# Optimization experiments

Measured on AMD Instinct MI355X. Metric: run time of the kernel, lower is better.

Reference implementation:

```python
import jax, jax.numpy as jnp
import numpy as np

H = 128
W = 128
TILE = 32
N = 12000
BIG = 1e30


def _render(means2D, cov2d, color, opacity, depths):
    # pixel coords, indexing='xy': pix[y, x] = (x, y)
    pix = jnp.stack(jnp.meshgrid(jnp.arange(W), jnp.arange(H), indexing='xy'), axis=-1).astype(means2D.dtype)
    c00 = cov2d[:, 0, 0]; c01 = cov2d[:, 0, 1]; c10 = cov2d[:, 1, 0]; c11 = cov2d[:, 1, 1]
    det = c00 * c11 - c01 * c10
    # get_radius (no_grad in torch)
    mid = 0.5 * (c00 + c11)
    s = jnp.sqrt(jnp.maximum(mid * mid - det, 0.1))
    radii = jax.lax.stop_gradient(3.0 * jnp.ceil(jnp.sqrt(jnp.maximum(mid + s, mid - s))))
    # get_rect, clipped to image bounds
    rmin = jnp.clip(means2D - radii[:, None], 0.0, W - 1.0)  # H == W == 128
    rmax = jnp.clip(means2D + radii[:, None], 0.0, W - 1.0)
    rmin = jax.lax.stop_gradient(rmin)
    rmax = jax.lax.stop_gradient(rmax)
    # closed-form 2x2 inverse (conic)
    inv_det = 1.0 / det
    conic = jnp.stack([jnp.stack([c11, -c01], axis=-1),
                       jnp.stack([-c10, c00], axis=-1)], axis=-2) * inv_det[:, None, None]

    img_c = jnp.ones((H, W, 3), means2D.dtype)
    img_d = jnp.zeros((H, W, 1), means2D.dtype)
    img_a = jnp.zeros((H, W, 1), means2D.dtype)

    for h in range(0, H, TILE):
        for w in range(0, W, TILE):
            tlx = jnp.maximum(rmin[:, 0], w); tly = jnp.maximum(rmin[:, 1], h)
            brx = jnp.minimum(rmax[:, 0], w + TILE - 1.0); bry = jnp.minimum(rmax[:, 1], h + TILE - 1.0)
            mask = (brx > tlx) & (bry > tly)  # [N]
            # depth sort with non-intersecting gaussians pushed to the back
            order = jnp.argsort(jnp.where(mask, depths, BIG))
            sm = means2D[order]          # [N,2]
            sc = conic[order]            # [N,2,2]
            so = opacity[order]          # [N,1]
            scol = color[order]          # [N,3]
            smask = mask[order]
            sd = jnp.where(smask, depths[order], 0.0)
            tile_coord = pix[h:h + TILE, w:w + TILE].reshape(-1, 2)  # [1024,2]
            dx = tile_coord[:, None, :] - sm[None]                   # [1024,N,2]
            gw = jnp.exp(-0.5 * (dx[..., 0] ** 2 * sc[:, 0, 0]
                                 + dx[..., 1] ** 2 * sc[:, 1, 1]
                                 + dx[..., 0] * dx[..., 1] * (sc[:, 0, 1] + sc[:, 1, 0])))
            alpha = gw[..., None] * so[None] * smask[None, :, None].astype(gw.dtype)  # [1024,N,1]
            alpha = jnp.minimum(alpha, 0.99)
            T = jnp.cumprod(jnp.concatenate([jnp.ones_like(alpha[:, :1]), 1.0 - alpha[:, :-1]], axis=1), axis=1)
            wgt = T * alpha
            acc = wgt.sum(axis=1)                                   # [1024,1]
            tc = (wgt * scol[None]).sum(axis=1) + (1.0 - acc)       # white background
            td = (wgt * sd[None, :, None]).sum(axis=1)
            img_c = img_c.at[h:h + TILE, w:w + TILE].set(tc.reshape(TILE, TILE, 3))
            img_d = img_d.at[h:h + TILE, w:w + TILE].set(td.reshape(TILE, TILE, 1))
            img_a = img_a.at[h:h + TILE, w:w + TILE].set(acc.reshape(TILE, TILE, 1))
    return img_c, img_d, img_a


def setup_inputs() -> dict:
    key = jax.random.key(0)
    k1, k2, k3, k4, k5 = jax.random.split(key, 5)
    means2D = jax.random.uniform(k1, (N, 2), jnp.float32) * 128.0
    L = 0.6 * jax.random.normal(k2, (N, 2, 2), jnp.float32)
    cov2d = L @ jnp.swapaxes(L, -1, -2) + 0.3 * jnp.eye(2, dtype=jnp.float32)[None]
    color = jax.random.uniform(k3, (N, 3), jnp.float32)
    opacity = jax.random.uniform(k4, (N, 1), jnp.float32)
    depths = jax.random.uniform(k5, (N,), jnp.float32) * 10.0 + 0.2
    return {"means2D": means2D, "cov2d": cov2d, "color": color, "opacity": opacity, "depths": depths}


def reference(means2D, cov2d, color, opacity, depths):
    return _render(means2D, cov2d, color, opacity, depths)
```

## Files before the change

kernel.cpp:

```cpp
#include <hip/hip_runtime.h>
#include <stdint.h>

#define HH 128
#define WW 128
#define NTILES 16
#define NPIX (HH * WW)
#define MAXSEG 16
#define JCH 1024

__global__ void k0_init(const float* __restrict__ depths,
                        uint64_t* __restrict__ keys,
                        int* __restrict__ rank, int N) {
    int i = blockIdx.x * blockDim.x + threadIdx.x;
    if (i < N) {
        rank[i] = 0;
        keys[i] = ((uint64_t)__float_as_uint(depths[i]) << 32) | (uint64_t)i;
    }
}

__global__ __launch_bounds__(256) void k1_rank(const uint64_t* __restrict__ keys,
                                               int* __restrict__ rank,
                                               int N, int ncj) {
    int bi = blockIdx.x / ncj;
    int bj = blockIdx.x % ncj;
    int t  = threadIdx.x;
    int i  = bi * 256 + t;
    uint64_t ki = (i < N) ? keys[i] : 0;

    int j0   = bj * JCH;
    int jend = min(N, j0 + JCH);

    int c0 = 0, c1 = 0, c2 = 0, c3 = 0;
    int j = j0;
    for (; j + 4 <= jend; j += 4) {
        uint64_t a = keys[j + 0];
        uint64_t b = keys[j + 1];
        uint64_t c = keys[j + 2];
        uint64_t d = keys[j + 3];
        c0 += (a < ki);
        c1 += (b < ki);
        c2 += (c < ki);
        c3 += (d < ki);
    }
    for (; j < jend; j++) c0 += (keys[j] < ki);

    if (i < N) {
        int cnt = (c0 + c1) + (c2 + c3);
        if (cnt) atomicAdd(&rank[i], cnt);
    }
}

__global__ __launch_bounds__(256) void k2_scatter(const float* __restrict__ means,
                                                  const float* __restrict__ cov,
                                                  const float* __restrict__ color,
                                                  const float* __restrict__ opac,
                                                  const float* __restrict__ depths,
                                                  const int* __restrict__ rank,
                                                  float* __restrict__ sorted,
                                                  int* __restrict__ smask,
                                                  int N) {
    int i = blockIdx.x * blockDim.x + threadIdx.x;
    if (i >= N) return;

    float mx = means[2 * i + 0];
    float my = means[2 * i + 1];
    float c00 = cov[4 * i + 0];
    float c01 = cov[4 * i + 1];
    float c10 = cov[4 * i + 2];
    float c11 = cov[4 * i + 3];

    float det = c00 * c11 - c01 * c10;
    float mid = 0.5f * (c00 + c11);
    float s = sqrtf(fmaxf(mid * mid - det, 0.1f));
    float radii = 3.0f * ceilf(sqrtf(fmaxf(mid + s, mid - s)));

    float rminx = fminf(fmaxf(mx - radii, 0.0f), (float)(WW - 1));
    float rminy = fminf(fmaxf(my - radii, 0.0f), (float)(HH - 1));
    float rmaxx = fminf(fmaxf(mx + radii, 0.0f), (float)(WW - 1));
    float rmaxy = fminf(fmaxf(my + radii, 0.0f), (float)(HH - 1));

    float inv_det = 1.0f / det;
    float A = c11 * inv_det;
    float B = c00 * inv_det;
    float C = -(c01 + c10) * inv_det;

    int bits = 0;
    for (int ty = 0; ty < 4; ty++) {
        float h = (float)(ty * 32);
        float tly = fmaxf(rminy, h);
        float bry = fminf(rmaxy, h + 31.0f);
        bool yok = bry > tly;
        for (int tx = 0; tx < 4; tx++) {
            float w = (float)(tx * 32);
            float tlx = fmaxf(rminx, w);
            float brx = fminf(rmaxx, w + 31.0f);
            if (yok && (brx > tlx)) bits |= 1 << (ty * 4 + tx);
        }
    }

    int r = rank[i];
    float4* g4 = (float4*)(sorted + (size_t)r * 12);
    g4[0] = make_float4(mx, my, A, B);
    g4[1] = make_float4(C, opac[i], color[3 * i + 0], color[3 * i + 1]);
    g4[2] = make_float4(color[3 * i + 2], depths[i], 0.0f, 0.0f);
    smask[r] = bits;
}

__global__ __launch_bounds__(256) void k3_compact(const int* __restrict__ smask,
                                                  int* __restrict__ lists,
                                                  int* __restrict__ counts,
                                                  int N) {
    int tile = blockIdx.x;
    int t = threadIdx.x;
    int lane = t & 63;
    int wv = t >> 6;

    __shared__ int wsum[4];
    __shared__ int s_run;
    if (t == 0) s_run = 0;
    __syncthreads();

    int* list = lists + (size_t)tile * N;

    for (int base = 0; base < N; base += 256) {
        int idx = base + t;
        int flag = (idx < N) ? ((smask[idx] >> tile) & 1) : 0;
        unsigned long long bal = __ballot(flag);
        int pre = __popcll(bal & ((lane == 0) ? 0ull : ((1ull << lane) - 1ull)));
        int wtot = __popcll(bal);
        if (lane == 0) wsum[wv] = wtot;
        __syncthreads();
        int woff = 0;
        for (int q = 0; q < wv; q++) woff += wsum[q];
        int run = s_run;
        if (flag) list[run + woff + pre] = idx;
        __syncthreads();
        if (t == 0) s_run = run + wsum[0] + wsum[1] + wsum[2] + wsum[3];
        __syncthreads();
    }
    if (t == 0) counts[tile] = s_run;
}

#define CH 64
__global__ __launch_bounds__(256) void k4_render(const float* __restrict__ sorted,
                                                 const int* __restrict__ lists,
                                                 const int* __restrict__ counts,
                                                 float4* __restrict__ part4,
                                                 float2* __restrict__ part2,
                                                 int N, int S) {
    int b = blockIdx.x;
    int s = b & (S - 1);
    int q = b / S;
    int tile = q >> 2;
    int sub = q & 3;
    int tx = tile & 3;
    int ty = tile >> 2;
    int t = threadIdx.x;

    int p = sub * 256 + t;
    int px = p & 31;
    int py = p >> 5;
    float fx = (float)(tx * 32 + px);
    float fy = (float)(ty * 32 + py);

    int cnt = counts[tile];
    int chunk = (cnt + S - 1) / S;
    int beg = s * chunk;
    int end = min(cnt, beg + chunk);
    const int* list = lists + (size_t)tile * N;

    __shared__ __align__(16) float4 s_g[CH * 3];
    __shared__ int s_idx[CH];

    float T = 1.0f;
    float ar = 0.0f, ag = 0.0f, ab = 0.0f, ad = 0.0f, aa = 0.0f;

    for (int base = beg; base < end; base += CH) {
        int m = min(CH, end - base);
        if (t < CH) s_idx[t] = (t < m) ? list[base + t] : 0;
        __syncthreads();
        if (t < m * 3) {
            int k = t / 3;
            int c = t - k * 3;
            s_g[t] = ((const float4*)(sorted + (size_t)s_idx[k] * 12))[c];
        }
        __syncthreads();
        for (int k = 0; k < m; k++) {
            float4 ga = s_g[k * 3 + 0];
            float4 gb = s_g[k * 3 + 1];
            float4 gc = s_g[k * 3 + 2];
            float dx = fx - ga.x;
            float dy = fy - ga.y;
            float e = ga.z * dx * dx + ga.w * dy * dy + gb.x * dx * dy;
            float gw = __expf(-0.5f * e);
            float alpha = fminf(gw * gb.y, 0.99f);
            float w = T * alpha;
            ar += w * gb.z;
            ag += w * gb.w;
            ab += w * gc.x;
            ad += w * gc.y;
            aa += w;
            T *= (1.0f - alpha);
        }
        __syncthreads();
    }

    size_t o = (size_t)s * NPIX + (size_t)tile * 1024 + p;
    part4[o] = make_float4(ar, ag, ab, ad);
    part2[o] = make_float2(aa, T);
}

__global__ __launch_bounds__(256) void k5_combine(const float4* __restrict__ part4,
                                                  const float2* __restrict__ part2,
                                                  float* __restrict__ out, int S) {
    int pid = blockIdx.x * 256 + threadIdx.x;
    int tile = pid >> 10;
    int p = pid & 1023;
    int px = p & 31;
    int py = p >> 5;
    int gx = (tile & 3) * 32 + px;
    int gy = (tile >> 2) * 32 + py;

    float T = 1.0f;
    float ar = 0.0f, ag = 0.0f, ab = 0.0f, ad = 0.0f, aa = 0.0f;
    for (int s = 0; s < S; s++) {
        float4 q4 = part4[(size_t)s * NPIX + pid];
        float2 q2 = part2[(size_t)s * NPIX + pid];
        ar += T * q4.x;
        ag += T * q4.y;
        ab += T * q4.z;
        ad += T * q4.w;
        aa += T * q2.x;
        T *= q2.y;
    }

    int pidx = gy * WW + gx;
    float bgr = 1.0f - aa;
    out[pidx * 3 + 0] = ar + bgr;
    out[pidx * 3 + 1] = ag + bgr;
    out[pidx * 3 + 2] = ab + bgr;
    out[HH * WW * 3 + pidx] = ad;
    out[HH * WW * 4 + pidx] = aa;
}

extern "C" void kernel_launch(void* const* d_in, const int* in_sizes, int n_in,
                              void* d_out, int out_size, void* d_ws, size_t ws_size,
                              hipStream_t stream) {
    const float* means  = (const float*)d_in[0];
    const float* cov    = (const float*)d_in[1];
    const float* color  = (const float*)d_in[2];
    const float* opac   = (const float*)d_in[3];
    const float* depths = (const float*)d_in[4];
    float* out = (float*)d_out;

    int N = in_sizes[4];
    size_t NA = ((size_t)N + 255) / 256 * 256;

    size_t o_rank   = 0;
    size_t o_keys   = o_rank + NA * 4;
    size_t o_sorted = o_keys + NA * 8;
    size_t o_smask  = o_sorted + NA * 48;
    size_t o_lists  = o_smask + NA * 4;
    size_t o_counts = o_lists + (size_t)NTILES * NA * 4;
    size_t o_part4  = o_counts + 256;

    int S = 1;
    while (S < MAXSEG &&
           o_part4 + (size_t)(S * 2) * NPIX * 24 <= ws_size) S *= 2;
    size_t o_part2 = o_part4 + (size_t)S * NPIX * 16;

    int*      rank     = (int*)((char*)d_ws + o_rank);
    uint64_t* keys     = (uint64_t*)((char*)d_ws + o_keys);
    float*    sorted   = (float*)((char*)d_ws + o_sorted);
    int*      smask    = (int*)((char*)d_ws + o_smask);
    int*      lists    = (int*)((char*)d_ws + o_lists);
    int*      counts   = (int*)((char*)d_ws + o_counts);
    float4*   part4    = (float4*)((char*)d_ws + o_part4);
    float2*   part2    = (float2*)((char*)d_ws + o_part2);

    int nb  = (N + 255) / 256;
    int ncj = (N + JCH - 1) / JCH;

    k0_init<<<nb, 256, 0, stream>>>(depths, keys, rank, N);
    k1_rank<<<nb * ncj, 256, 0, stream>>>(keys, rank, N, ncj);
    k2_scatter<<<nb, 256, 0, stream>>>(means, cov, color, opac, depths, rank,
                                       sorted, smask, N);
    k3_compact<<<NTILES, 256, 0, stream>>>(smask, lists, counts, N);
    k4_render<<<64 * S, 256, 0, stream>>>(sorted, lists, counts, part4, part2,
                                          N, S);
    k5_combine<<<NPIX / 256, 256, 0, stream>>>(part4, part2, out, S);
}
```

Before: 143.1 us.

## Drop init kernel, replace rank atomics with partial sums, widen compaction blocks

Removes the key-init kernel by building sort keys on the fly from depths inside the rank kernel. Each column chunk now writes its count to a per-chunk partial buffer instead of doing atomicAdd, and the scatter kernel sums those partials. The chunk size is halved to give more blocks, and the compaction kernel uses 1024-thread blocks with a shared prefix over 16 waves, so it needs fewer serial iterations. Trade-offs are more partial-sum reads per element in the scatter kernel and more key construction work inside the inner loop.

Result: faster. 140.1 us (-2.1%).

```diff
diff --git a/kernel.cpp b/kernel.cpp
--- a/kernel.cpp
+++ b/kernel.cpp
@@ -6,26 +6,21 @@
 #define NTILES 16
 #define NPIX (HH * WW)
 #define MAXSEG 16
-#define JCH 1024
-
-__global__ void k0_init(const float* __restrict__ depths,
-                        uint64_t* __restrict__ keys,
-                        int* __restrict__ rank, int N) {
-    int i = blockIdx.x * blockDim.x + threadIdx.x;
-    if (i < N) {
-        rank[i] = 0;
-        keys[i] = ((uint64_t)__float_as_uint(depths[i]) << 32) | (uint64_t)i;
-    }
-}
-
-__global__ __launch_bounds__(256) void k1_rank(const uint64_t* __restrict__ keys,
-                                               int* __restrict__ rank,
-                                               int N, int ncj) {
+#define JCH 512
+
+__device__ __forceinline__ uint64_t mkkey(float d, int i) {
+    return ((uint64_t)__float_as_uint(d) << 32) | (uint64_t)(uint32_t)i;
+}
+
+__global__ __launch_bounds__(256) void k1_rank(const float* __restrict__ depths,
+                                               int* __restrict__ part,
+                                               int N, int ncj, int NA) {
     int bi = blockIdx.x / ncj;
     int bj = blockIdx.x % ncj;
     int t  = threadIdx.x;
     int i  = bi * 256 + t;
-    uint64_t ki = (i < N) ? keys[i] : 0;
+    float di = (i < N) ? depths[i] : 0.0f;
+    uint64_t ki = mkkey(di, i);
 
     int j0   = bj * JCH;
     int jend = min(N, j0 + JCH);
@@ -33,21 +28,18 @@
     int c0 = 0, c1 = 0, c2 = 0, c3 = 0;
     int j = j0;
     for (; j + 4 <= jend; j += 4) {
-        uint64_t a = keys[j + 0];
-        uint64_t b = keys[j + 1];
-        uint64_t c = keys[j + 2];
-        uint64_t d = keys[j + 3];
+        uint64_t a = mkkey(depths[j + 0], j + 0);
+        uint64_t b = mkkey(depths[j + 1], j + 1);
+        uint64_t c = mkkey(depths[j + 2], j + 2);
+        uint64_t d = mkkey(depths[j + 3], j + 3);
         c0 += (a < ki);
         c1 += (b < ki);
         c2 += (c < ki);
         c3 += (d < ki);
     }
-    for (; j < jend; j++) c0 += (keys[j] < ki);
-
-    if (i < N) {
-        int cnt = (c0 + c1) + (c2 + c3);
-        if (cnt) atomicAdd(&rank[i], cnt);
-    }
+    for (; j < jend; j++) c0 += (mkkey(depths[j], j) < ki);
+
+    if (i < N) part[(size_t)bj * NA + i] = (c0 + c1) + (c2 + c3);
 }
 
 __global__ __launch_bounds__(256) void k2_scatter(const float* __restrict__ means,
@@ -55,12 +47,15 @@
                                                   const float* __restrict__ color,
                                                   const float* __restrict__ opac,
                                                   const float* __restrict__ depths,
-                                                  const int* __restrict__ rank,
+                                                  const int* __restrict__ part,
                                                   float* __restrict__ sorted,
                                                   int* __restrict__ smask,
-                                                  int N) {
+                                                  int N, int ncj, int NA) {
     int i = blockIdx.x * blockDim.x + threadIdx.x;
     if (i >= N) return;
+
+    int r = 0;
+    for (int b = 0; b < ncj; b++) r += part[(size_t)b * NA + i];
 
     float mx = means[2 * i + 0];
     float my = means[2 * i + 1];
@@ -98,7 +93,6 @@
         }
     }
 
-    int r = rank[i];
     float4* g4 = (float4*)(sorted + (size_t)r * 12);
     g4[0] = make_float4(mx, my, A, B);
     g4[1] = make_float4(C, opac[i], color[3 * i + 0], color[3 * i + 1]);
@@ -106,36 +100,40 @@
     smask[r] = bits;
 }
 
-__global__ __launch_bounds__(256) void k3_compact(const int* __restrict__ smask,
-                                                  int* __restrict__ lists,
-                                                  int* __restrict__ counts,
-                                                  int N) {
+__global__ __launch_bounds__(1024) void k3_compact(const int* __restrict__ smask,
+                                                   int* __restrict__ lists,
+                                                   int* __restrict__ counts,
+                                                   int N) {
     int tile = blockIdx.x;
     int t = threadIdx.x;
     int lane = t & 63;
     int wv = t >> 6;
 
-    __shared__ int wsum[4];
+    __shared__ int wsum[16];
+    __shared__ int woff[16];
     __shared__ int s_run;
     if (t == 0) s_run = 0;
     __syncthreads();
 
     int* list = lists + (size_t)tile * N;
 
-    for (int base = 0; base < N; base += 256) {
+    for (int base = 0; base < N; base += 1024) {
         int idx = base + t;
         int flag = (idx < N) ? ((smask[idx] >> tile) & 1) : 0;
         unsigned long long bal = __ballot(flag);
-        int pre = __popcll(bal & ((lane == 0) ? 0ull : ((1ull << lane) - 1ull)));
-        int wtot = __popcll(bal);
-        if (lane == 0) wsum[wv] = wtot;
-        __syncthreads();
-        int woff = 0;
-        for (int q = 0; q < wv; q++) woff += wsum[q];
+        int pre = __popcll(bal & ((1ull << lane) - 1ull));
+        if (lane == 63) wsum[wv] = pre + flag;
+        __syncthreads();
+        if (wv == 0 && lane < 16) {
+            int v = 0;
+            for (int q = 0; q < lane; q++) v += wsum[q];
+            woff[lane] = v;
+        }
+        __syncthreads();
         int run = s_run;
-        if (flag) list[run + woff + pre] = idx;
-        __syncthreads();
-        if (t == 0) s_run = run + wsum[0] + wsum[1] + wsum[2] + wsum[3];
+        if (flag) list[run + woff[wv] + pre] = idx;
+        __syncthreads();
+        if (t == 0) s_run = run + woff[15] + wsum[15];
         __syncthreads();
     }
     if (t == 0) counts[tile] = s_run;
@@ -254,13 +252,14 @@
     float* out = (float*)d_out;
 
     int N = in_sizes[4];
-    size_t NA = ((size_t)N + 255) / 256 * 256;
-
-    size_t o_rank   = 0;
-    size_t o_keys   = o_rank + NA * 4;
-    size_t o_sorted = o_keys + NA * 8;
-    size_t o_smask  = o_sorted + NA * 48;
-    size_t o_lists  = o_smask + NA * 4;
+    int NA = (int)(((size_t)N + 255) / 256 * 256);
+    int nb  = (N + 255) / 256;
+    int ncj = (N + JCH - 1) / JCH;
+
+    size_t o_part   = 0;
+    size_t o_sorted = o_part + (size_t)ncj * NA * 4;
+    size_t o_smask  = o_sorted + (size_t)NA * 48;
+    size_t o_lists  = o_smask + (size_t)NA * 4;
     size_t o_counts = o_lists + (size_t)NTILES * NA * 4;
     size_t o_part4  = o_counts + 256;
 
@@ -269,23 +268,18 @@
            o_part4 + (size_t)(S * 2) * NPIX * 24 <= ws_size) S *= 2;
     size_t o_part2 = o_part4 + (size_t)S * NPIX * 16;
 
-    int*      rank     = (int*)((char*)d_ws + o_rank);
-    uint64_t* keys     = (uint64_t*)((char*)d_ws + o_keys);
-    float*    sorted   = (float*)((char*)d_ws + o_sorted);
-    int*      smask    = (int*)((char*)d_ws + o_smask);
-    int*      lists    = (int*)((char*)d_ws + o_lists);
-    int*      counts   = (int*)((char*)d_ws + o_counts);
-    float4*   part4    = (float4*)((char*)d_ws + o_part4);
-    float2*   part2    = (float2*)((char*)d_ws + o_part2);
-
-    int nb  = (N + 255) / 256;
-    int ncj = (N + JCH - 1) / JCH;
-
-    k0_init<<<nb, 256, 0, stream>>>(depths, keys, rank, N);
-    k1_rank<<<nb * ncj, 256, 0, stream>>>(keys, rank, N, ncj);
-    k2_scatter<<<nb, 256, 0, stream>>>(means, cov, color, opac, depths, rank,
-                                       sorted, smask, N);
-    k3_compact<<<NTILES, 256, 0, stream>>>(smask, lists, counts, N);
+    int*    part   = (int*)((char*)d_ws + o_part);
+    float*  sorted = (float*)((char*)d_ws + o_sorted);
+    int*    smask  = (int*)((char*)d_ws + o_smask);
+    int*    lists  = (int*)((char*)d_ws + o_lists);
+    int*    counts = (int*)((char*)d_ws + o_counts);
+    float4* part4  = (float4*)((char*)d_ws + o_part4);
+    float2* part2  = (float2*)((char*)d_ws + o_part2);
+
+    k1_rank<<<nb * ncj, 256, 0, stream>>>(depths, part, N, ncj, NA);
+    k2_scatter<<<nb, 256, 0, stream>>>(means, cov, color, opac, depths, part,
+                                       sorted, smask, N, ncj, NA);
+    k3_compact<<<NTILES, 1024, 0, stream>>>(smask, lists, counts, N);
     k4_render<<<64 * S, 256, 0, stream>>>(sorted, lists, counts, part4, part2,
                                           N, S);
     k5_combine<<<NPIX / 256, 256, 0, stream>>>(part4, part2, out, S);
```
